# Optimization experiments

Hardware: AMD Instinct MI355X
Metric: run time of the kernel (lower is better)

## Reference

```python
import jax, jax.numpy as jnp
import numpy as np

B, S, D, H = 4, 2048, 1024, 16
HD = D // H  # head_dim = 64


def setup_inputs() -> dict:
    key = jax.random.key(0)
    ks = jax.random.split(key, 5)
    scale = 1.0 / np.sqrt(D)
    return {
        "x": jax.random.normal(ks[0], (B, S, D), dtype=jnp.float32),
        "Wq": jax.random.normal(ks[1], (D, D), dtype=jnp.float32) * scale,
        "bq": jnp.zeros((D,), dtype=jnp.float32),
        "Wk": jax.random.normal(ks[2], (D, D), dtype=jnp.float32) * scale,
        "bk": jnp.zeros((D,), dtype=jnp.float32),
        "Wv": jax.random.normal(ks[3], (D, D), dtype=jnp.float32) * scale,
        "bv": jnp.zeros((D,), dtype=jnp.float32),
        "Wo": jax.random.normal(ks[4], (D, D), dtype=jnp.float32) * scale,
        "bo": jnp.zeros((D,), dtype=jnp.float32),
    }


def reference(x, Wq, bq, Wk, bk, Wv, bv, Wo, bo):
    # Linear layers (torch Linear: y = x @ W^T + b)
    q = jnp.einsum("bsd,ed->bse", x, Wq) + bq
    k = jnp.einsum("bsd,ed->bse", x, Wk) + bk
    v = jnp.einsum("bsd,ed->bse", x, Wv) + bv
    # split heads -> [B, H, S, HD]
    q = q.reshape(B, S, H, HD).transpose(0, 2, 1, 3)
    k = k.reshape(B, S, H, HD).transpose(0, 2, 1, 3)
    v = v.reshape(B, S, H, HD).transpose(0, 2, 1, 3)
    # NOTE: original scales by 1/sqrt(d_model), not 1/sqrt(head_dim)
    scores = jnp.einsum("bhqd,bhkd->bhqk", q, k) / jnp.sqrt(jnp.float32(D))
    causal = jnp.tril(jnp.ones((S, S), dtype=bool))
    scores = jnp.where(causal, scores, -jnp.inf)
    probs = jax.nn.softmax(scores, axis=-1)  # dropout p=0 -> identity
    attn = jnp.einsum("bhqk,bhkd->bhqd", probs, v)
    # merge heads -> [B, S, D]
    attn = attn.transpose(0, 2, 1, 3).reshape(B, S, D)
    out = jnp.einsum("bsd,ed->bse", attn, Wo) + bo
    return out
```

## Files before the change

kernel.cpp:

```cpp
#include <hip/hip_runtime.h>
#include <hip/hip_bf16.h>
#include <stdint.h>
#include <stddef.h>

#define B_N 4
#define S_N 2048
#define D_N 1024
#define H_N 16
#define HD_N 64

typedef __bf16 bf16;
typedef __bf16 bf16x8 __attribute__((ext_vector_type(8)));
typedef __bf16 bf16x4 __attribute__((ext_vector_type(4)));
typedef float f32x4 __attribute__((ext_vector_type(4)));

__device__ __forceinline__ void gload_lds16(const void* g, void* l) {
  __builtin_amdgcn_global_load_lds((const __attribute__((address_space(1))) void*)g,
                                   (__attribute__((address_space(3))) void*)l,
                                   16, 0, 0);
}

__global__ __launch_bounds__(256) void cvt_f32_bf16(const float* __restrict__ in,
                                                    bf16* __restrict__ out, int n4) {
  int i = blockIdx.x * blockDim.x + threadIdx.x;
  const int stride = gridDim.x * blockDim.x;
  for (; i < n4; i += stride) {
    const float4 v = ((const float4*)in)[i];
    bf16x4 o;
    o[0] = (bf16)v.x; o[1] = (bf16)v.y; o[2] = (bf16)v.z; o[3] = (bf16)v.w;
    ((bf16x4*)out)[i] = o;
  }
}

__global__ __launch_bounds__(256) void cvt_w4(const float* __restrict__ w0,
                                              const float* __restrict__ w1,
                                              const float* __restrict__ w2,
                                              const float* __restrict__ w3,
                                              bf16* __restrict__ o0, bf16* __restrict__ o1,
                                              bf16* __restrict__ o2, bf16* __restrict__ o3) {
  const int n4 = (D_N * D_N) / 4;
  const int which = blockIdx.x >> 9;
  const float* in = which == 0 ? w0 : which == 1 ? w1 : which == 2 ? w2 : w3;
  bf16* out = which == 0 ? o0 : which == 1 ? o1 : which == 2 ? o2 : o3;
  int i = (blockIdx.x & 511) * 256 + threadIdx.x;
  const int stride = 512 * 256;
  for (; i < n4; i += stride) {
    const float4 v = ((const float4*)in)[i];
    bf16x4 o;
    o[0] = (bf16)v.x; o[1] = (bf16)v.y; o[2] = (bf16)v.z; o[3] = (bf16)v.w;
    ((bf16x4*)out)[i] = o;
  }
}

__global__ __launch_bounds__(256, 2) void gemm_qkv3(const bf16* __restrict__ A,
                                                    const bf16* __restrict__ Wq,
                                                    const bf16* __restrict__ Wk,
                                                    const bf16* __restrict__ Wv,
                                                    const float* __restrict__ bq,
                                                    const float* __restrict__ bk,
                                                    const float* __restrict__ bv,
                                                    bf16* __restrict__ outQ,
                                                    bf16* __restrict__ outK,
                                                    bf16* __restrict__ outVt) {
  __shared__ __align__(16) char smem[2 * 32768];
  const int tid = threadIdx.x;
  const int wid = tid >> 6;
  const int lane = tid & 63;
  const int l16 = lane & 15;
  const int lhi = lane >> 4;
  const int n0 = blockIdx.x * 128;
  const int m0 = blockIdx.y * 128;

  const int wm = (wid >> 1) * 64;
  const int wn = (wid & 1) * 64;
  const int srow4 = lane >> 2;
  const int scol = 8 * ((lane & 3) ^ (srow4 & 3));
  const int rswz = (lhi ^ (l16 & 3)) * 16;

  f32x4 acc[3][4][4];
#pragma unroll
  for (int w = 0; w < 3; ++w)
#pragma unroll
    for (int i = 0; i < 4; ++i)
#pragma unroll
      for (int j = 0; j < 4; ++j) acc[w][i][j] = (f32x4){0.f, 0.f, 0.f, 0.f};

#define STG(buf_, kt_)                                                                    \
  {                                                                                       \
    _Pragma("unroll") for (int q = 0; q < 2; ++q)                                         \
        gload_lds16(A + (size_t)(m0 + q * 64 + wid * 16 + srow4) * D_N + (kt_)*32 + scol, \
                    smem + (buf_)*32768 + q * 4096 + wid * 1024);                         \
    _Pragma("unroll") for (int q = 0; q < 2; ++q) {                                       \
      gload_lds16(Wq + (size_t)(n0 + q * 64 + wid * 16 + srow4) * D_N + (kt_)*32 + scol,  \
                  smem + (buf_)*32768 + 8192 + q * 4096 + wid * 1024);                    \
      gload_lds16(Wk + (size_t)(n0 + q * 64 + wid * 16 + srow4) * D_N + (kt_)*32 + scol,  \
                  smem + (buf_)*32768 + 16384 + q * 4096 + wid * 1024);                   \
      gload_lds16(Wv + (size_t)(n0 + q * 64 + wid * 16 + srow4) * D_N + (kt_)*32 + scol,  \
                  smem + (buf_)*32768 + 24576 + q * 4096 + wid * 1024);                   \
    }                                                                                     \
  }

#define PHASE(buf_)                                                                       \
  {                                                                                       \
    const char* a_ = smem + (buf_)*32768;                                                 \
    const char* b_ = a_ + 8192;                                                           \
    bf16x8 af[4];                                                                         \
    _Pragma("unroll") for (int i = 0; i < 4; ++i)                                         \
        af[i] = *(const bf16x8*)(a_ + (wm + i * 16 + l16) * 64 + rswz);                   \
    _Pragma("unroll") for (int w = 0; w < 3; ++w) {                                       \
      bf16x8 bfr[4];                                                                      \
      _Pragma("unroll") for (int j = 0; j < 4; ++j)                                       \
          bfr[j] = *(const bf16x8*)(b_ + (w * 128 + wn + j * 16 + l16) * 64 + rswz);      \
      __builtin_amdgcn_s_setprio(1);                                                      \
      _Pragma("unroll") for (int i = 0; i < 4; ++i)                                       \
          _Pragma("unroll") for (int j = 0; j < 4; ++j)                                   \
              acc[w][i][j] = __builtin_amdgcn_mfma_f32_16x16x32_bf16(af[i], bfr[j],       \
                                                                     acc[w][i][j], 0, 0, 0); \
      __builtin_amdgcn_s_setprio(0);                                                      \
    }                                                                                     \
  }

  const int NT = D_N / 32;

  STG(0, 0);
  STG(1, 1);
  asm volatile("s_waitcnt vmcnt(8)" ::: "memory");
  asm volatile("s_barrier" ::: "memory");

  for (int t = 0; t < NT - 2; ++t) {
    const int cur = t & 1;
    PHASE(cur);
    asm volatile("s_barrier" ::: "memory");
    STG(cur, t + 2);
    asm volatile("s_waitcnt vmcnt(8)" ::: "memory");
    asm volatile("s_barrier" ::: "memory");
  }
  PHASE(0);
  asm volatile("s_waitcnt vmcnt(0)" ::: "memory");
  asm volatile("s_barrier" ::: "memory");
  PHASE(1);

#undef STG
#undef PHASE

#pragma unroll
  for (int w = 0; w < 3; ++w) {
    const float* bias = w == 0 ? bq : w == 1 ? bk : bv;
#pragma unroll
    for (int i = 0; i < 4; ++i) {
#pragma unroll
      for (int j = 0; j < 4; ++j) {
        const int row0 = m0 + wm + i * 16 + lhi * 4;
        const int col = n0 + wn + j * 16 + l16;
        const float bvv = bias[col];
        const int h = col >> 6, hd = col & 63;
        if (w == 2) {
          const int b = row0 >> 11, s = row0 & (S_N - 1);
          bf16x4 pk;
#pragma unroll
          for (int r = 0; r < 4; ++r) pk[r] = (bf16)(acc[w][i][j][r] + bvv);
          *(bf16x4*)&outVt[(((size_t)b * H_N + h) * HD_N + hd) * S_N + s] = pk;
        } else {
          bf16* out = w == 0 ? outQ : outK;
#pragma unroll
          for (int r = 0; r < 4; ++r) {
            const int row = row0 + r;
            const int b = row >> 11, s = row & (S_N - 1);
            out[(((size_t)b * H_N + h) * S_N + s) * HD_N + hd] = (bf16)(acc[w][i][j][r] + bvv);
          }
        }
      }
    }
  }
}

__global__ __launch_bounds__(256, 3) void gemm_out(const bf16* __restrict__ A,
                                                   const bf16* __restrict__ W,
                                                   const float* __restrict__ bias,
                                                   float* __restrict__ out) {
  __shared__ __align__(16) char smem[2 * 16384];
  const int tid = threadIdx.x;
  const int wid = tid >> 6;
  const int lane = tid & 63;
  const int l16 = lane & 15;
  const int lhi = lane >> 4;
  const int n0 = blockIdx.x * 128;
  const int m0 = blockIdx.y * 128;

  const int wm = (wid >> 1) * 64;
  const int wn = (wid & 1) * 64;
  const int srow4 = lane >> 2;
  const int scol = 8 * ((lane & 3) ^ (srow4 & 3));
  const int rswz = (lhi ^ (l16 & 3)) * 16;

  f32x4 acc[4][4];
#pragma unroll
  for (int i = 0; i < 4; ++i)
#pragma unroll
    for (int j = 0; j < 4; ++j) acc[i][j] = (f32x4){0.f, 0.f, 0.f, 0.f};

#define STG(buf_, kt_)                                                                    \
  {                                                                                       \
    _Pragma("unroll") for (int q = 0; q < 2; ++q) {                                       \
      gload_lds16(A + (size_t)(m0 + q * 64 + wid * 16 + srow4) * D_N + (kt_)*32 + scol,   \
                  smem + (buf_)*16384 + q * 4096 + wid * 1024);                           \
      gload_lds16(W + (size_t)(n0 + q * 64 + wid * 16 + srow4) * D_N + (kt_)*32 + scol,   \
                  smem + (buf_)*16384 + 8192 + q * 4096 + wid * 1024);                    \
    }                                                                                     \
  }

#define PHASE(buf_)                                                                       \
  {                                                                                       \
    const char* a_ = smem + (buf_)*16384;                                                 \
    const char* b_ = a_ + 8192;                                                           \
    bf16x8 af[4], bfr[4];                                                                 \
    _Pragma("unroll") for (int i = 0; i < 4; ++i)                                         \
        af[i] = *(const bf16x8*)(a_ + (wm + i * 16 + l16) * 64 + rswz);                   \
    _Pragma("unroll") for (int j = 0; j < 4; ++j)                                         \
        bfr[j] = *(const bf16x8*)(b_ + (wn + j * 16 + l16) * 64 + rswz);                  \
    __builtin_amdgcn_s_setprio(1);                                                        \
    _Pragma("unroll") for (int i = 0; i < 4; ++i)                                         \
        _Pragma("unroll") for (int j = 0; j < 4; ++j)                                     \
            acc[i][j] = __builtin_amdgcn_mfma_f32_16x16x32_bf16(af[i], bfr[j],            \
                                                                acc[i][j], 0, 0, 0);      \
    __builtin_amdgcn_s_setprio(0);                                                        \
  }

  const int NT = D_N / 32;

  STG(0, 0);
  STG(1, 1);
  asm volatile("s_waitcnt vmcnt(4)" ::: "memory");
  asm volatile("s_barrier" ::: "memory");

  for (int t = 0; t < NT - 2; ++t) {
    const int cur = t & 1;
    PHASE(cur);
    asm volatile("s_barrier" ::: "memory");
    STG(cur, t + 2);
    asm volatile("s_waitcnt vmcnt(4)" ::: "memory");
    asm volatile("s_barrier" ::: "memory");
  }
  PHASE(0);
  asm volatile("s_waitcnt vmcnt(0)" ::: "memory");
  asm volatile("s_barrier" ::: "memory");
  PHASE(1);

#undef STG
#undef PHASE

#pragma unroll
  for (int i = 0; i < 4; ++i) {
#pragma unroll
    for (int j = 0; j < 4; ++j) {
      const int row0 = m0 + wm + i * 16 + lhi * 4;
      const int col = n0 + wn + j * 16 + l16;
      const float bvv = bias[col];
#pragma unroll
      for (int r = 0; r < 4; ++r) out[(size_t)(row0 + r) * D_N + col] = acc[i][j][r] + bvv;
    }
  }
}

__global__ __launch_bounds__(256, 3) void attn_fwd(const bf16* __restrict__ Q,
                                                   const bf16* __restrict__ K,
                                                   const bf16* __restrict__ Vt,
                                                   bf16* __restrict__ O) {
  __shared__ __align__(16) bf16 sK[2][64 * 64];
  __shared__ __align__(16) bf16 sV[2][64 * 64];
  __shared__ __align__(16) bf16 sP[4][32 * 72];
  const int tid = threadIdx.x;
  const int wave = tid >> 6;
  const int lane = tid & 63;
  const int l16 = lane & 15;
  const int lhi = lane >> 4;
  const int bidx = blockIdx.x;
  const int bh = bidx & 63;
  const int qt = 15 - (bidx >> 6);
  const int q0 = qt * 128 + wave * 32;
  const bf16* Qh = Q + (size_t)bh * S_N * HD_N;
  const bf16* Kh = K + (size_t)bh * S_N * HD_N;
  const bf16* Vth = Vt + (size_t)bh * HD_N * S_N;
  const int b = bh >> 4, h = bh & 15;

  const int srow = lane >> 3;
  const int scol = 8 * ((lane & 7) ^ srow);

  const float QS = 0.03125f * 1.44269504088896340736f;
  const f32x4 z4 = {0.0f, 0.0f, 0.0f, 0.0f};
  const f32x4 m4 = {-4.0f, -4.0f, -4.0f, -4.0f};
  const bf16 oneb = (bf16)1.0f;
  const bf16x8 ones = {oneb, oneb, oneb, oneb, oneb, oneb, oneb, oneb};
  bf16* sPw = sP[wave];

  bf16x8 qf[2][2];
#pragma unroll
  for (int i = 0; i < 2; ++i)
#pragma unroll
    for (int kq = 0; kq < 2; ++kq) {
      const bf16x8 raw =
          *(const bf16x8*)&Qh[(size_t)(q0 + i * 16 + l16) * HD_N + kq * 32 + lhi * 8];
      bf16x8 s;
#pragma unroll
      for (int e = 0; e < 8; ++e) s[e] = (bf16)((float)raw[e] * QS);
      qf[i][kq] = s;
    }

  f32x4 o[2][4];
  f32x4 osum[2];
#pragma unroll
  for (int i = 0; i < 2; ++i) {
#pragma unroll
    for (int j = 0; j < 4; ++j) o[i][j] = z4;
    osum[i] = z4;
  }

#define STAGE(buf, kb_)                                                                  \
  {                                                                                      \
    _Pragma("unroll") for (int is = 0; is < 2; ++is) {                                   \
      const int r0 = is * 32 + wave * 8;                                                 \
      gload_lds16(Kh + (size_t)((kb_)*64 + r0 + srow) * HD_N + scol, &sK[buf][r0 * 64]); \
      gload_lds16(Vth + (size_t)(r0 + srow) * S_N + (kb_)*64 + scol, &sV[buf][r0 * 64]); \
    }                                                                                    \
  }

  const int nkb = 2 * qt + 2;

  STAGE(0, 0);
  __syncthreads();

  for (int kb = 0; kb < nkb; ++kb) {
    const int cur = kb & 1;
    if (kb + 1 < nkb) STAGE(cur ^ 1, kb + 1);
    const bf16* sKb = sK[cur];
    const bf16* sVb = sV[cur];
    const int k0 = kb * 64;

    if (k0 <= q0 + 31) {
      f32x4 sc[2][4];
#pragma unroll
      for (int i = 0; i < 2; ++i)
#pragma unroll
        for (int j = 0; j < 4; ++j) sc[i][j] = m4;
      __builtin_amdgcn_s_setprio(1);
#pragma unroll
      for (int j = 0; j < 4; ++j) {
        const int row = j * 16 + l16;
#pragma unroll
        for (int kq = 0; kq < 2; ++kq) {
          const bf16x8 kfr = *(const bf16x8*)((const char*)sKb + row * 128 +
                                              ((kq * 64 + lhi * 16) ^ ((row & 7) << 4)));
#pragma unroll
          for (int i = 0; i < 2; ++i)
            sc[i][j] = __builtin_amdgcn_mfma_f32_16x16x32_bf16(qf[i][kq], kfr, sc[i][j], 0, 0, 0);
        }
      }
      __builtin_amdgcn_s_setprio(0);

      if (k0 + 63 > q0) {
#pragma unroll
        for (int i = 0; i < 2; ++i)
#pragma unroll
          for (int r = 0; r < 4; ++r) {
            const int qrow = q0 + i * 16 + lhi * 4 + r;
#pragma unroll
            for (int j = 0; j < 4; ++j)
              if (k0 + j * 16 + l16 > qrow) sc[i][j][r] = -3e38f;
          }
      }

#pragma unroll
      for (int i = 0; i < 2; ++i)
#pragma unroll
        for (int r = 0; r < 4; ++r)
#pragma unroll
          for (int j = 0; j < 4; ++j)
            sPw[(i * 16 + lhi * 4 + r) * 72 + j * 16 + l16] =
                (bf16)__builtin_amdgcn_exp2f(sc[i][j][r]);

      __builtin_amdgcn_s_setprio(1);
#pragma unroll
      for (int kq = 0; kq < 2; ++kq) {
        bf16x8 pa[2];
#pragma unroll
        for (int i = 0; i < 2; ++i)
          pa[i] = *(const bf16x8*)&sPw[(i * 16 + l16) * 72 + kq * 32 + lhi * 8];
#pragma unroll
        for (int i = 0; i < 2; ++i)
          osum[i] = __builtin_amdgcn_mfma_f32_16x16x32_bf16(pa[i], ones, osum[i], 0, 0, 0);
#pragma unroll
        for (int jd = 0; jd < 4; ++jd) {
          const int vrow = jd * 16 + l16;
          const bf16x8 vb = *(const bf16x8*)((const char*)sVb + vrow * 128 +
                                             ((kq * 64 + lhi * 16) ^ ((vrow & 7) << 4)));
#pragma unroll
          for (int i = 0; i < 2; ++i)
            o[i][jd] = __builtin_amdgcn_mfma_f32_16x16x32_bf16(pa[i], vb, o[i][jd], 0, 0, 0);
        }
      }
      __builtin_amdgcn_s_setprio(0);
    }
    __syncthreads();
  }

#pragma unroll
  for (int i = 0; i < 2; ++i) {
#pragma unroll
    for (int r = 0; r < 4; ++r) {
      const float inv = __builtin_amdgcn_rcpf(osum[i][r]);
      const size_t token = (size_t)b * S_N + q0 + i * 16 + lhi * 4 + r;
#pragma unroll
      for (int jd = 0; jd < 4; ++jd) {
        const int col = h * 64 + jd * 16 + l16;
        O[token * D_N + col] = (bf16)(o[i][jd][r] * inv);
      }
    }
  }
#undef STAGE
}

extern "C" void kernel_launch(void* const* d_in, const int* in_sizes, int n_in,
                              void* d_out, int out_size, void* d_ws, size_t ws_size,
                              hipStream_t stream) {
  const float* x  = (const float*)d_in[0];
  const float* Wq = (const float*)d_in[1];
  const float* bq = (const float*)d_in[2];
  const float* Wk = (const float*)d_in[3];
  const float* bk = (const float*)d_in[4];
  const float* Wv = (const float*)d_in[5];
  const float* bv = (const float*)d_in[6];
  const float* Wo = (const float*)d_in[7];
  const float* bo = (const float*)d_in[8];

  char* ws = (char*)d_ws;
  const size_t MB = 1u << 20;
  bf16* xb  = (bf16*)(ws);
  bf16* qB  = (bf16*)(ws + 16 * MB);
  bf16* kB  = (bf16*)(ws + 32 * MB);
  bf16* vtB = (bf16*)(ws + 48 * MB);
  bf16* wqb = (bf16*)(ws + 64 * MB);
  bf16* wkb = (bf16*)(ws + 66 * MB);
  bf16* wvb = (bf16*)(ws + 68 * MB);
  bf16* wob = (bf16*)(ws + 70 * MB);

  cvt_f32_bf16<<<2048, 256, 0, stream>>>(x, xb, (B_N * S_N * D_N) / 4);
  cvt_w4<<<2048, 256, 0, stream>>>(Wq, Wk, Wv, Wo, wqb, wkb, wvb, wob);

  gemm_qkv3<<<dim3(8, 64), 256, 0, stream>>>(xb, wqb, wkb, wvb, bq, bk, bv, qB, kB, vtB);

  attn_fwd<<<dim3(1024), 256, 0, stream>>>(qB, kB, vtB, xb);

  gemm_out<<<dim3(8, 64), 256, 0, stream>>>(xb, wob, bo, (float*)d_out);
}
```

Baseline: 155.0 us.

## Fuse x fp32-to-bf16 conversion into QKV GEMM A-tile staging

Drops the separate cvt_f32_bf16 kernel and has the QKV GEMM read x in fp32 directly. A tiles are loaded into registers a stage ahead, converted to bf16 and written to swizzled LDS, while the weight tiles keep their direct global-to-LDS loads. The goal is to skip one kernel launch and the 32 MB write and re-read of the bf16 copy of x. In exchange every GEMM block now reads twice as many bytes for A, and the register prefetch with hand-set waitcnt values adds pressure and ordering risk.

```diff
diff --git a/kernel.cpp b/kernel.cpp
--- a/kernel.cpp
+++ b/kernel.cpp
@@ -18,18 +18,6 @@
   __builtin_amdgcn_global_load_lds((const __attribute__((address_space(1))) void*)g,
                                    (__attribute__((address_space(3))) void*)l,
                                    16, 0, 0);
-}
-
-__global__ __launch_bounds__(256) void cvt_f32_bf16(const float* __restrict__ in,
-                                                    bf16* __restrict__ out, int n4) {
-  int i = blockIdx.x * blockDim.x + threadIdx.x;
-  const int stride = gridDim.x * blockDim.x;
-  for (; i < n4; i += stride) {
-    const float4 v = ((const float4*)in)[i];
-    bf16x4 o;
-    o[0] = (bf16)v.x; o[1] = (bf16)v.y; o[2] = (bf16)v.z; o[3] = (bf16)v.w;
-    ((bf16x4*)out)[i] = o;
-  }
 }
 
 __global__ __launch_bounds__(256) void cvt_w4(const float* __restrict__ w0,
@@ -52,7 +40,7 @@
   }
 }
 
-__global__ __launch_bounds__(256, 2) void gemm_qkv3(const bf16* __restrict__ A,
+__global__ __launch_bounds__(256, 2) void gemm_qkv3(const float* __restrict__ X,
                                                     const bf16* __restrict__ Wq,
                                                     const bf16* __restrict__ Wk,
                                                     const bf16* __restrict__ Wv,
@@ -85,11 +73,29 @@
 #pragma unroll
       for (int j = 0; j < 4; ++j) acc[w][i][j] = (f32x4){0.f, 0.f, 0.f, 0.f};
 
-#define STG(buf_, kt_)                                                                    \
-  {                                                                                       \
-    _Pragma("unroll") for (int q = 0; q < 2; ++q)                                         \
-        gload_lds16(A + (size_t)(m0 + q * 64 + wid * 16 + srow4) * D_N + (kt_)*32 + scol, \
-                    smem + (buf_)*32768 + q * 4096 + wid * 1024);                         \
+  float4 arA[2][2], arB[2][2];
+
+#define ALOAD(AR, kt_)                                                                    \
+  {                                                                                       \
+    _Pragma("unroll") for (int q = 0; q < 2; ++q) {                                       \
+      const float* p_ = X + (size_t)(m0 + q * 64 + wid * 16 + srow4) * D_N + (kt_)*32 + scol; \
+      AR[q][0] = *(const float4*)p_;                                                      \
+      AR[q][1] = *(const float4*)(p_ + 4);                                                \
+    }                                                                                     \
+  }
+#define AWRITE(buf_, AR)                                                                  \
+  {                                                                                       \
+    _Pragma("unroll") for (int q = 0; q < 2; ++q) {                                       \
+      bf16x8 w_;                                                                          \
+      w_[0] = (bf16)AR[q][0].x; w_[1] = (bf16)AR[q][0].y;                                 \
+      w_[2] = (bf16)AR[q][0].z; w_[3] = (bf16)AR[q][0].w;                                 \
+      w_[4] = (bf16)AR[q][1].x; w_[5] = (bf16)AR[q][1].y;                                 \
+      w_[6] = (bf16)AR[q][1].z; w_[7] = (bf16)AR[q][1].w;                                 \
+      *(bf16x8*)(smem + (buf_)*32768 + q * 4096 + wid * 1024 + lane * 16) = w_;           \
+    }                                                                                     \
+  }
+#define STG_W(buf_, kt_)                                                                  \
+  {                                                                                       \
     _Pragma("unroll") for (int q = 0; q < 2; ++q) {                                       \
       gload_lds16(Wq + (size_t)(n0 + q * 64 + wid * 16 + srow4) * D_N + (kt_)*32 + scol,  \
                   smem + (buf_)*32768 + 8192 + q * 4096 + wid * 1024);                    \
@@ -120,27 +126,43 @@
     }                                                                                     \
   }
 
-  const int NT = D_N / 32;
-
-  STG(0, 0);
-  STG(1, 1);
-  asm volatile("s_waitcnt vmcnt(8)" ::: "memory");
+#define ITER(t_, ARW, ARL)                                                                \
+  {                                                                                       \
+    PHASE((t_)&1);                                                                        \
+    asm volatile("s_barrier" ::: "memory");                                               \
+    STG_W((t_)&1, (t_) + 2);                                                              \
+    asm volatile("s_waitcnt vmcnt(6)" ::: "memory");                                      \
+    AWRITE((t_)&1, ARW);                                                                  \
+    if ((t_) + 3 < 32) ALOAD(ARL, (t_) + 3);                                              \
+    asm volatile("s_waitcnt lgkmcnt(0)" ::: "memory");                                    \
+    asm volatile("s_barrier" ::: "memory");                                               \
+  }
+
+  ALOAD(arA, 0);
+  STG_W(0, 0);
+  ALOAD(arB, 1);
+  STG_W(1, 1);
+  asm volatile("s_waitcnt vmcnt(16)" ::: "memory");
+  AWRITE(0, arA);
+  asm volatile("s_waitcnt vmcnt(6)" ::: "memory");
+  AWRITE(1, arB);
+  ALOAD(arA, 2);
+  asm volatile("s_waitcnt lgkmcnt(0)" ::: "memory");
   asm volatile("s_barrier" ::: "memory");
 
-  for (int t = 0; t < NT - 2; ++t) {
-    const int cur = t & 1;
-    PHASE(cur);
-    asm volatile("s_barrier" ::: "memory");
-    STG(cur, t + 2);
-    asm volatile("s_waitcnt vmcnt(8)" ::: "memory");
-    asm volatile("s_barrier" ::: "memory");
+  for (int t = 0; t < 30; t += 2) {
+    ITER(t, arA, arB);
+    ITER(t + 1, arB, arA);
   }
   PHASE(0);
   asm volatile("s_waitcnt vmcnt(0)" ::: "memory");
   asm volatile("s_barrier" ::: "memory");
   PHASE(1);
 
-#undef STG
+#undef ITER
+#undef ALOAD
+#undef AWRITE
+#undef STG_W
 #undef PHASE
 
 #pragma unroll
@@ -443,10 +465,9 @@
   bf16* wvb = (bf16*)(ws + 68 * MB);
   bf16* wob = (bf16*)(ws + 70 * MB);
 
-  cvt_f32_bf16<<<2048, 256, 0, stream>>>(x, xb, (B_N * S_N * D_N) / 4);
   cvt_w4<<<2048, 256, 0, stream>>>(Wq, Wk, Wv, Wo, wqb, wkb, wvb, wob);
 
-  gemm_qkv3<<<dim3(8, 64), 256, 0, stream>>>(xb, wqb, wkb, wvb, bq, bk, bv, qB, kB, vtB);
+  gemm_qkv3<<<dim3(8, 64), 256, 0, stream>>>(x, wqb, wkb, wvb, bq, bk, bv, qB, kB, vtB);
 
   attn_fwd<<<dim3(1024), 256, 0, stream>>>(qB, kB, vtB, xb);
 
```

Measured after the change: 253.9 us. 63.8% more time.
